# Optimization experiments

Hardware: AMD Instinct MI355X
Metric: run time of the kernel (lower is better)

The kernel has to match this reference:

```python
import jax, jax.numpy as jnp
import numpy as np

B, N, C, K = 1024, 100, 256, 3  # batch, num_proposals, hidden_dim, conv kernel size
LN_EPS = 1e-5


def setup_inputs() -> dict:
    key = jax.random.key(0)
    k1, k2, k3 = jax.random.split(key, 3)
    query = jax.random.normal(k1, (B, N, C), dtype=jnp.float32)
    value = jax.random.normal(k2, (B, N, C), dtype=jnp.float32)
    # weight_linear: Linear(hidden_dim -> kernel_size)
    W_w = jax.random.normal(k3, (K, C), dtype=jnp.float32) * (1.0 / np.sqrt(C))
    b_w = jnp.zeros((K,), dtype=jnp.float32)
    # LayerNorm(hidden_dim)
    gamma = jnp.ones((C,), dtype=jnp.float32)
    beta = jnp.zeros((C,), dtype=jnp.float32)
    return {"query": query, "value": value, "W_w": W_w, "b_w": b_w,
            "gamma": gamma, "beta": beta}


def reference(query, value, W_w, b_w, gamma, beta):
    Bq, Nq, Cq = query.shape
    Kk = W_w.shape[0]
    # dynamic depthwise kernels: [B, N, K]
    w = jnp.einsum('bnc,kc->bnk', query, W_w) + b_w
    # torch conv1d with padding='same' (cross-correlation along C, groups=N)
    pad_l = (Kk - 1) // 2
    pad_r = Kk // 2
    vpad = jnp.pad(value, ((0, 0), (0, 0), (pad_l, pad_r)))
    # sliding windows along channel axis: [B, N, C, K]
    win = jnp.stack([vpad[:, :, k:k + Cq] for k in range(Kk)], axis=-1)
    out = jnp.einsum('bnck,bnk->bnc', win, w)
    # LayerNorm over last dim
    mu = jnp.mean(out, axis=-1, keepdims=True)
    var = jnp.mean(jnp.square(out - mu), axis=-1, keepdims=True)
    out = (out - mu) * jax.lax.rsqrt(var + LN_EPS) * gamma + beta
    return out
```

## Files before the change

kernel.cpp:

```cpp
#include <hip/hip_runtime.h>

constexpr int B = 1024, N = 100, C = 256, K = 3;
constexpr int ROWS = B * N;
constexpr int WAVES_PER_BLOCK = 4;
constexpr int BLOCKS = ROWS / WAVES_PER_BLOCK;
constexpr float LN_EPS = 1e-5f;

__global__ __launch_bounds__(256) void dydwconv_ln_kernel(
    const float* __restrict__ query,
    const float* __restrict__ value,
    const float* __restrict__ Ww,
    const float* __restrict__ bw,
    const float* __restrict__ gamma,
    const float* __restrict__ beta,
    float* __restrict__ out)
{
    __shared__ float sW[K * C];
    __shared__ float sGamma[C];
    __shared__ float sBeta[C];
    __shared__ float sBw[K];

    const int t = threadIdx.x;
    sW[t]         = Ww[t];
    sW[t + C]     = Ww[t + C];
    sW[t + 2 * C] = Ww[t + 2 * C];
    sGamma[t] = gamma[t];
    sBeta[t]  = beta[t];
    if (t < K) sBw[t] = bw[t];
    __syncthreads();

    const int wave = t >> 6;
    const int lane = t & 63;
    const int row  = blockIdx.x * WAVES_PER_BLOCK + wave;

    const size_t base = (size_t)row * C + lane * 4;
    const float4 q4 = *(const float4*)(query + base);
    const float4 v4 = *(const float4*)(value + base);

    const int c0 = lane * 4;
    float p0 = q4.x * sW[c0]         + q4.y * sW[c0 + 1]         + q4.z * sW[c0 + 2]         + q4.w * sW[c0 + 3];
    float p1 = q4.x * sW[C + c0]     + q4.y * sW[C + c0 + 1]     + q4.z * sW[C + c0 + 2]     + q4.w * sW[C + c0 + 3];
    float p2 = q4.x * sW[2*C + c0]   + q4.y * sW[2*C + c0 + 1]   + q4.z * sW[2*C + c0 + 2]   + q4.w * sW[2*C + c0 + 3];

    #pragma unroll
    for (int off = 32; off > 0; off >>= 1) {
        p0 += __shfl_xor(p0, off);
        p1 += __shfl_xor(p1, off);
        p2 += __shfl_xor(p2, off);
    }
    const float w0 = p0 + sBw[0];
    const float w1 = p1 + sBw[1];
    const float w2 = p2 + sBw[2];

    float vleft  = __shfl_up(v4.w, 1);
    float vright = __shfl_down(v4.x, 1);
    if (lane == 0)  vleft  = 0.0f;
    if (lane == 63) vright = 0.0f;

    const float o0 = vleft * w0 + v4.x * w1 + v4.y * w2;
    const float o1 = v4.x  * w0 + v4.y * w1 + v4.z * w2;
    const float o2 = v4.y  * w0 + v4.z * w1 + v4.w * w2;
    const float o3 = v4.z  * w0 + v4.w * w1 + vright * w2;

    float s  = o0 + o1 + o2 + o3;
    float ss = o0 * o0 + o1 * o1 + o2 * o2 + o3 * o3;
    #pragma unroll
    for (int off = 32; off > 0; off >>= 1) {
        s  += __shfl_xor(s, off);
        ss += __shfl_xor(ss, off);
    }
    const float mu  = s * (1.0f / C);
    const float var = ss * (1.0f / C) - mu * mu;
    const float inv = rsqrtf(var + LN_EPS);

    float4 r;
    r.x = (o0 - mu) * inv * sGamma[c0]     + sBeta[c0];
    r.y = (o1 - mu) * inv * sGamma[c0 + 1] + sBeta[c0 + 1];
    r.z = (o2 - mu) * inv * sGamma[c0 + 2] + sBeta[c0 + 2];
    r.w = (o3 - mu) * inv * sGamma[c0 + 3] + sBeta[c0 + 3];
    *(float4*)(out + base) = r;
}

extern "C" void kernel_launch(void* const* d_in, const int* in_sizes, int n_in,
                              void* d_out, int out_size, void* d_ws, size_t ws_size,
                              hipStream_t stream) {
    const float* query = (const float*)d_in[0];
    const float* value = (const float*)d_in[1];
    const float* Ww    = (const float*)d_in[2];
    const float* bw    = (const float*)d_in[3];
    const float* gamma = (const float*)d_in[4];
    const float* beta  = (const float*)d_in[5];
    float* out = (float*)d_out;

    dydwconv_ln_kernel<<<BLOCKS, 256, 0, stream>>>(query, value, Ww, bw, gamma, beta, out);
}
```

Baseline: 252.9 us.

## Map 16 lanes per row with DPP reductions, drop LDS staging, nontemporal stores

Reassigns work so each row is handled by 16 lanes, each holding four float4 chunks, which raises per-thread memory parallelism and cuts the block count. Wave-wide shuffle reductions become 16-lane DPP row rotations, and the halo exchange uses DPP shifts with wraparound between chunks. Shared-memory staging of the weights, gamma and beta, along with the block barrier, is removed in favour of direct cached global loads. The output is written with nontemporal stores to avoid polluting the cache. Register pressure rises in exchange.

```diff
diff --git a/kernel.cpp b/kernel.cpp
--- a/kernel.cpp
+++ b/kernel.cpp
@@ -2,9 +2,31 @@
 
 constexpr int B = 1024, N = 100, C = 256, K = 3;
 constexpr int ROWS = B * N;
-constexpr int WAVES_PER_BLOCK = 4;
-constexpr int BLOCKS = ROWS / WAVES_PER_BLOCK;
+constexpr int THREADS = 256;
+constexpr int LANES_PER_ROW = 16;
+constexpr int ROWS_PER_BLOCK = THREADS / LANES_PER_ROW;
+constexpr int BLOCKS = ROWS / ROWS_PER_BLOCK;
 constexpr float LN_EPS = 1e-5f;
+
+typedef float f32x4 __attribute__((ext_vector_type(4)));
+
+#define DPP_ROW_SHL(n) (0x100 | (n))
+#define DPP_ROW_SHR(n) (0x110 | (n))
+#define DPP_ROW_ROR(n) (0x120 | (n))
+
+template <int CTRL, bool BOUND_ZERO>
+__device__ __forceinline__ float fdpp(float x) {
+    return __int_as_float(__builtin_amdgcn_update_dpp(
+        0, __float_as_int(x), CTRL, 0xF, 0xF, BOUND_ZERO));
+}
+
+__device__ __forceinline__ float rowsum16(float x) {
+    x += fdpp<DPP_ROW_ROR(1), false>(x);
+    x += fdpp<DPP_ROW_ROR(2), false>(x);
+    x += fdpp<DPP_ROW_ROR(4), false>(x);
+    x += fdpp<DPP_ROW_ROR(8), false>(x);
+    return x;
+}
 
 __global__ __launch_bounds__(256) void dydwconv_ln_kernel(
     const float* __restrict__ query,
@@ -15,70 +37,80 @@
     const float* __restrict__ beta,
     float* __restrict__ out)
 {
-    __shared__ float sW[K * C];
-    __shared__ float sGamma[C];
-    __shared__ float sBeta[C];
-    __shared__ float sBw[K];
+    const int t = threadIdx.x;
+    const int l = t & 15;
+    const int row = blockIdx.x * ROWS_PER_BLOCK + (t >> 4);
+    const size_t base = (size_t)row * C;
 
-    const int t = threadIdx.x;
-    sW[t]         = Ww[t];
-    sW[t + C]     = Ww[t + C];
-    sW[t + 2 * C] = Ww[t + 2 * C];
-    sGamma[t] = gamma[t];
-    sBeta[t]  = beta[t];
-    if (t < K) sBw[t] = bw[t];
-    __syncthreads();
+    float4 q[4], v[4];
+    #pragma unroll
+    for (int j = 0; j < 4; ++j) {
+        const int c = (j * 16 + l) * 4;
+        q[j] = *(const float4*)(query + base + c);
+        v[j] = *(const float4*)(value + base + c);
+    }
 
-    const int wave = t >> 6;
-    const int lane = t & 63;
-    const int row  = blockIdx.x * WAVES_PER_BLOCK + wave;
+    float p0 = 0.f, p1 = 0.f, p2 = 0.f;
+    #pragma unroll
+    for (int j = 0; j < 4; ++j) {
+        const int c = (j * 16 + l) * 4;
+        const float4 a = *(const float4*)(Ww + c);
+        const float4 b = *(const float4*)(Ww + C + c);
+        const float4 d = *(const float4*)(Ww + 2 * C + c);
+        p0 += q[j].x * a.x + q[j].y * a.y + q[j].z * a.z + q[j].w * a.w;
+        p1 += q[j].x * b.x + q[j].y * b.y + q[j].z * b.z + q[j].w * b.w;
+        p2 += q[j].x * d.x + q[j].y * d.y + q[j].z * d.z + q[j].w * d.w;
+    }
+    p0 = rowsum16(p0);
+    p1 = rowsum16(p1);
+    p2 = rowsum16(p2);
+    const float w0 = p0 + bw[0];
+    const float w1 = p1 + bw[1];
+    const float w2 = p2 + bw[2];
 
-    const size_t base = (size_t)row * C + lane * 4;
-    const float4 q4 = *(const float4*)(query + base);
-    const float4 v4 = *(const float4*)(value + base);
+    const bool is_l0  = (l == 0);
+    const bool is_l15 = (l == 15);
 
-    const int c0 = lane * 4;
-    float p0 = q4.x * sW[c0]         + q4.y * sW[c0 + 1]         + q4.z * sW[c0 + 2]         + q4.w * sW[c0 + 3];
-    float p1 = q4.x * sW[C + c0]     + q4.y * sW[C + c0 + 1]     + q4.z * sW[C + c0 + 2]     + q4.w * sW[C + c0 + 3];
-    float p2 = q4.x * sW[2*C + c0]   + q4.y * sW[2*C + c0 + 1]   + q4.z * sW[2*C + c0 + 2]   + q4.w * sW[2*C + c0 + 3];
-
+    float4 o[4];
+    float s = 0.f, ss = 0.f;
     #pragma unroll
-    for (int off = 32; off > 0; off >>= 1) {
-        p0 += __shfl_xor(p0, off);
-        p1 += __shfl_xor(p1, off);
-        p2 += __shfl_xor(p2, off);
+    for (int j = 0; j < 4; ++j) {
+        float vl = fdpp<DPP_ROW_SHR(1), true>(v[j].w);
+        if (j > 0) {
+            const float wrap = fdpp<DPP_ROW_ROR(1), false>(v[j - 1].w);
+            vl = is_l0 ? wrap : vl;
+        }
+        float vr = fdpp<DPP_ROW_SHL(1), true>(v[j].x);
+        if (j < 3) {
+            const float wrap = fdpp<DPP_ROW_ROR(15), false>(v[j + 1].x);
+            vr = is_l15 ? wrap : vr;
+        }
+        o[j].x = vl     * w0 + v[j].x * w1 + v[j].y * w2;
+        o[j].y = v[j].x * w0 + v[j].y * w1 + v[j].z * w2;
+        o[j].z = v[j].y * w0 + v[j].z * w1 + v[j].w * w2;
+        o[j].w = v[j].z * w0 + v[j].w * w1 + vr     * w2;
+        s  += (o[j].x + o[j].y) + (o[j].z + o[j].w);
+        ss += o[j].x * o[j].x + o[j].y * o[j].y
+            + o[j].z * o[j].z + o[j].w * o[j].w;
     }
-    const float w0 = p0 + sBw[0];
-    const float w1 = p1 + sBw[1];
-    const float w2 = p2 + sBw[2];
-
-    float vleft  = __shfl_up(v4.w, 1);
-    float vright = __shfl_down(v4.x, 1);
-    if (lane == 0)  vleft  = 0.0f;
-    if (lane == 63) vright = 0.0f;
-
-    const float o0 = vleft * w0 + v4.x * w1 + v4.y * w2;
-    const float o1 = v4.x  * w0 + v4.y * w1 + v4.z * w2;
-    const float o2 = v4.y  * w0 + v4.z * w1 + v4.w * w2;
-    const float o3 = v4.z  * w0 + v4.w * w1 + vright * w2;
-
-    float s  = o0 + o1 + o2 + o3;
-    float ss = o0 * o0 + o1 * o1 + o2 * o2 + o3 * o3;
-    #pragma unroll
-    for (int off = 32; off > 0; off >>= 1) {
-        s  += __shfl_xor(s, off);
-        ss += __shfl_xor(ss, off);
-    }
+    s  = rowsum16(s);
+    ss = rowsum16(ss);
     const float mu  = s * (1.0f / C);
     const float var = ss * (1.0f / C) - mu * mu;
     const float inv = rsqrtf(var + LN_EPS);
 
-    float4 r;
-    r.x = (o0 - mu) * inv * sGamma[c0]     + sBeta[c0];
-    r.y = (o1 - mu) * inv * sGamma[c0 + 1] + sBeta[c0 + 1];
-    r.z = (o2 - mu) * inv * sGamma[c0 + 2] + sBeta[c0 + 2];
-    r.w = (o3 - mu) * inv * sGamma[c0 + 3] + sBeta[c0 + 3];
-    *(float4*)(out + base) = r;
+    #pragma unroll
+    for (int j = 0; j < 4; ++j) {
+        const int c = (j * 16 + l) * 4;
+        const float4 g  = *(const float4*)(gamma + c);
+        const float4 bt = *(const float4*)(beta + c);
+        f32x4 r;
+        r.x = (o[j].x - mu) * inv * g.x + bt.x;
+        r.y = (o[j].y - mu) * inv * g.y + bt.y;
+        r.z = (o[j].z - mu) * inv * g.z + bt.z;
+        r.w = (o[j].w - mu) * inv * g.w + bt.w;
+        __builtin_nontemporal_store(r, (f32x4*)(out + base + c));
+    }
 }
 
 extern "C" void kernel_launch(void* const* d_in, const int* in_sizes, int n_in,
@@ -90,7 +122,8 @@
     const float* bw    = (const float*)d_in[3];
     const float* gamma = (const float*)d_in[4];
     const float* beta  = (const float*)d_in[5];
-    float* out = (float*)d_out;
+    float* outp = (float*)d_out;
 
-    dydwconv_ln_kernel<<<BLOCKS, 256, 0, stream>>>(query, value, Ww, bw, gamma, beta, out);
+    dydwconv_ln_kernel<<<BLOCKS, THREADS, 0, stream>>>(
+        query, value, Ww, bw, gamma, beta, outp);
 }
```

New measurement: 257.0 us. About the same (+1.6%).

## Use persistent grid-stride waves with register prefetch and DPP reductions

Applied to the files above, without the earlier changes.

Replaces the one-row-per-wave launch of 25600 blocks with a persistent grid of 2048 blocks. Each wave strides over rows and prefetches the next row's query and value into registers while computing the current row. Weights, gamma and beta move from shared memory into per-lane registers, which removes the LDS staging and the __syncthreads. The first four steps of each wave reduction use DPP row_ror instead of shuffles, and output stores are nontemporal. The aim is to amortize block launch and setup and hide load latency in this memory-bound kernel, at the cost of fewer resident waves to hide latency.

```diff
diff --git a/kernel.cpp b/kernel.cpp
--- a/kernel.cpp
+++ b/kernel.cpp
@@ -2,9 +2,29 @@
 
 constexpr int B = 1024, N = 100, C = 256, K = 3;
 constexpr int ROWS = B * N;
-constexpr int WAVES_PER_BLOCK = 4;
-constexpr int BLOCKS = ROWS / WAVES_PER_BLOCK;
+constexpr int THREADS = 256;
+constexpr int WAVES_PER_BLOCK = THREADS / 64;
+constexpr int BLOCKS = 2048;
+constexpr int TOTAL_WAVES = BLOCKS * WAVES_PER_BLOCK;
 constexpr float LN_EPS = 1e-5f;
+
+typedef float f32x4 __attribute__((ext_vector_type(4)));
+
+template <int N_>
+__device__ __forceinline__ float fror(float x) {
+    return __int_as_float(__builtin_amdgcn_update_dpp(
+        0, __float_as_int(x), 0x120 | N_, 0xF, 0xF, false));
+}
+
+__device__ __forceinline__ float wavesum(float x) {
+    x += fror<1>(x);
+    x += fror<2>(x);
+    x += fror<4>(x);
+    x += fror<8>(x);
+    x += __shfl_xor(x, 16);
+    x += __shfl_xor(x, 32);
+    return x;
+}
 
 __global__ __launch_bounds__(256) void dydwconv_ln_kernel(
     const float* __restrict__ query,
@@ -15,70 +35,71 @@
     const float* __restrict__ beta,
     float* __restrict__ out)
 {
-    __shared__ float sW[K * C];
-    __shared__ float sGamma[C];
-    __shared__ float sBeta[C];
-    __shared__ float sBw[K];
+    const int t    = threadIdx.x;
+    const int lane = t & 63;
+    const int c0   = lane * 4;
+    const int row0 = blockIdx.x * WAVES_PER_BLOCK + (t >> 6);
 
-    const int t = threadIdx.x;
-    sW[t]         = Ww[t];
-    sW[t + C]     = Ww[t + C];
-    sW[t + 2 * C] = Ww[t + 2 * C];
-    sGamma[t] = gamma[t];
-    sBeta[t]  = beta[t];
-    if (t < K) sBw[t] = bw[t];
-    __syncthreads();
+    const int nIter = (ROWS - row0 + TOTAL_WAVES - 1) / TOTAL_WAVES;
 
-    const int wave = t >> 6;
-    const int lane = t & 63;
-    const int row  = blockIdx.x * WAVES_PER_BLOCK + wave;
+    const float4 Wa = *(const float4*)(Ww + c0);
+    const float4 Wb = *(const float4*)(Ww + C + c0);
+    const float4 Wc = *(const float4*)(Ww + 2 * C + c0);
+    const float4 g4 = *(const float4*)(gamma + c0);
+    const float4 b4 = *(const float4*)(beta + c0);
+    const float  b0 = bw[0], b1 = bw[1], b2 = bw[2];
 
-    const size_t base = (size_t)row * C + lane * 4;
-    const float4 q4 = *(const float4*)(query + base);
-    const float4 v4 = *(const float4*)(value + base);
+    constexpr size_t STEP = (size_t)TOTAL_WAVES * C;
+    size_t off = (size_t)row0 * C + c0;
 
-    const int c0 = lane * 4;
-    float p0 = q4.x * sW[c0]         + q4.y * sW[c0 + 1]         + q4.z * sW[c0 + 2]         + q4.w * sW[c0 + 3];
-    float p1 = q4.x * sW[C + c0]     + q4.y * sW[C + c0 + 1]     + q4.z * sW[C + c0 + 2]     + q4.w * sW[C + c0 + 3];
-    float p2 = q4.x * sW[2*C + c0]   + q4.y * sW[2*C + c0 + 1]   + q4.z * sW[2*C + c0 + 2]   + q4.w * sW[2*C + c0 + 3];
+    float4 qc = *(const float4*)(query + off);
+    float4 vc = *(const float4*)(value + off);
 
-    #pragma unroll
-    for (int off = 32; off > 0; off >>= 1) {
-        p0 += __shfl_xor(p0, off);
-        p1 += __shfl_xor(p1, off);
-        p2 += __shfl_xor(p2, off);
+    for (int it = 0; it < nIter; ++it) {
+        const bool hn = (it + 1) < nIter;
+        const size_t noff = off + STEP;
+        float4 qn = qc, vn = vc;
+        if (hn) {
+            qn = *(const float4*)(query + noff);
+            vn = *(const float4*)(value + noff);
+        }
+
+        float p0 = qc.x * Wa.x + qc.y * Wa.y + qc.z * Wa.z + qc.w * Wa.w;
+        float p1 = qc.x * Wb.x + qc.y * Wb.y + qc.z * Wb.z + qc.w * Wb.w;
+        float p2 = qc.x * Wc.x + qc.y * Wc.y + qc.z * Wc.z + qc.w * Wc.w;
+        const float w0 = wavesum(p0) + b0;
+        const float w1 = wavesum(p1) + b1;
+        const float w2 = wavesum(p2) + b2;
+
+        float vl = __shfl_up(vc.w, 1);
+        float vr = __shfl_down(vc.x, 1);
+        if (lane == 0)  vl = 0.0f;
+        if (lane == 63) vr = 0.0f;
+
+        const float o0 = vl   * w0 + vc.x * w1 + vc.y * w2;
+        const float o1 = vc.x * w0 + vc.y * w1 + vc.z * w2;
+        const float o2 = vc.y * w0 + vc.z * w1 + vc.w * w2;
+        const float o3 = vc.z * w0 + vc.w * w1 + vr   * w2;
+
+        float s  = (o0 + o1) + (o2 + o3);
+        float ss = o0 * o0 + o1 * o1 + o2 * o2 + o3 * o3;
+        s  = wavesum(s);
+        ss = wavesum(ss);
+        const float mu  = s * (1.0f / C);
+        const float var = ss * (1.0f / C) - mu * mu;
+        const float inv = rsqrtf(var + LN_EPS);
+
+        f32x4 r;
+        r.x = (o0 - mu) * inv * g4.x + b4.x;
+        r.y = (o1 - mu) * inv * g4.y + b4.y;
+        r.z = (o2 - mu) * inv * g4.z + b4.z;
+        r.w = (o3 - mu) * inv * g4.w + b4.w;
+        __builtin_nontemporal_store(r, (f32x4*)(out + off));
+
+        off = noff;
+        qc = qn;
+        vc = vn;
     }
-    const float w0 = p0 + sBw[0];
-    const float w1 = p1 + sBw[1];
-    const float w2 = p2 + sBw[2];
-
-    float vleft  = __shfl_up(v4.w, 1);
-    float vright = __shfl_down(v4.x, 1);
-    if (lane == 0)  vleft  = 0.0f;
-    if (lane == 63) vright = 0.0f;
-
-    const float o0 = vleft * w0 + v4.x * w1 + v4.y * w2;
-    const float o1 = v4.x  * w0 + v4.y * w1 + v4.z * w2;
-    const float o2 = v4.y  * w0 + v4.z * w1 + v4.w * w2;
-    const float o3 = v4.z  * w0 + v4.w * w1 + vright * w2;
-
-    float s  = o0 + o1 + o2 + o3;
-    float ss = o0 * o0 + o1 * o1 + o2 * o2 + o3 * o3;
-    #pragma unroll
-    for (int off = 32; off > 0; off >>= 1) {
-        s  += __shfl_xor(s, off);
-        ss += __shfl_xor(ss, off);
-    }
-    const float mu  = s * (1.0f / C);
-    const float var = ss * (1.0f / C) - mu * mu;
-    const float inv = rsqrtf(var + LN_EPS);
-
-    float4 r;
-    r.x = (o0 - mu) * inv * sGamma[c0]     + sBeta[c0];
-    r.y = (o1 - mu) * inv * sGamma[c0 + 1] + sBeta[c0 + 1];
-    r.z = (o2 - mu) * inv * sGamma[c0 + 2] + sBeta[c0 + 2];
-    r.w = (o3 - mu) * inv * sGamma[c0 + 3] + sBeta[c0 + 3];
-    *(float4*)(out + base) = r;
 }
 
 extern "C" void kernel_launch(void* const* d_in, const int* in_sizes, int n_in,
@@ -90,7 +111,8 @@
     const float* bw    = (const float*)d_in[3];
     const float* gamma = (const float*)d_in[4];
     const float* beta  = (const float*)d_in[5];
-    float* out = (float*)d_out;
+    float* outp = (float*)d_out;
 
-    dydwconv_ln_kernel<<<BLOCKS, 256, 0, stream>>>(query, value, Ww, bw, gamma, beta, out);
+    dydwconv_ln_kernel<<<BLOCKS, THREADS, 0, stream>>>(
+        query, value, Ww, bw, gamma, beta, outp);
 }
```

Measured after the change: 262.6 us. +3.8%, slower.
